# Optimization experiments

Hardware: AMD Instinct MI355X
Metric: run time of the kernel (lower is better)

## Reference

```python
import jax, jax.numpy as jnp
from jax import lax
import numpy as np

N_T = 70            # linspace(0, 60, 70) RK4 grid
STATE_DIM = 12
NOISE_STD = 0.01
T0 = jnp.linspace(0.0, 60.0, N_T)
DEFAULT_TIMES = jnp.array([0, 2, 4, 6, 8, 10, 12, 14, 16, 18, 20, 25, 30, 40, 50, 60], dtype=jnp.float32)
EPORA_DATA = jnp.array([0.01713, 0.145, 0.2442, 0.7659, 1.0, 0.8605, 0.7829, 0.5705,
                        0.6217, 0.331, 0.3388, 0.3116, 0.05062, 0.02504, 0.01163, 0.01163], dtype=jnp.float32)
PARAM_SHIFT = jnp.array([0.5, 0.05, 4.0], dtype=jnp.float32)
PARAM_SCALE = jnp.array([2.5, 0.15, 6.0], dtype=jnp.float32)


def _deriv(x, k1, k2, tau, E):
    # x: [B, 12]; k1,k2,tau: [B]; E: scalar EpoRA(t)
    x1, x2, x3 = x[:, 0], x[:, 1], x[:, 2]
    q1, q2, q3, q4, q5, q6, q7, out = (x[:, 4], x[:, 5], x[:, 6], x[:, 7],
                                       x[:, 8], x[:, 9], x[:, 10], x[:, 11])
    r = 8.0 / tau
    return jnp.stack([
        -k1 * x1 * E + k2 * out,
        -x2 * x2 + k1 * x1 * E,
        -k2 * x3 + x2 * x2,
        -k2 * out + k2 * x3,
        r * (x3 - q1),
        r * (q1 - q2),
        r * (q2 - q3),
        r * (q3 - q4),
        r * (q4 - q5),
        r * (q5 - q6),
        r * (q6 - q7),
        r * (q7 - out),
    ], axis=1)


def _simulate(ps):
    # ps: [B, 3] transformed parameters -> trajectory [N_T, B, 12]
    B = ps.shape[0]
    k1, k2, tau = ps[:, 0], ps[:, 1], ps[:, 2]
    dt = T0[1] - T0[0]
    t_start = T0[:-1]
    # EpoRA is a function of t only: precompute at the 3 RK4 stage times per step
    e_lo = jnp.interp(t_start, DEFAULT_TIMES, EPORA_DATA)
    e_mid = jnp.interp(t_start + 0.5 * dt, DEFAULT_TIMES, EPORA_DATA)
    e_hi = jnp.interp(t_start + dt, DEFAULT_TIMES, EPORA_DATA)
    x0 = jnp.zeros((B, STATE_DIM), dtype=ps.dtype).at[:, 0].set(3.71)

    def step(x, es):
        ea, eb, ec = es
        s1 = _deriv(x, k1, k2, tau, ea)
        s2 = _deriv(x + 0.5 * dt * s1, k1, k2, tau, eb)
        s3 = _deriv(x + 0.5 * dt * s2, k1, k2, tau, eb)
        s4 = _deriv(x + dt * s3, k1, k2, tau, ec)
        xn = x + (dt / 6.0) * (s1 + 2.0 * s2 + 2.0 * s3 + s4)
        return xn, xn

    _, traj = lax.scan(step, x0, (e_lo, e_mid, e_hi))
    return jnp.concatenate([x0[None], traj], axis=0)  # [70, B, 12]


def _forward(parameters, design):
    ps = PARAM_SHIFT + jax.scipy.stats.norm.cdf(parameters) * PARAM_SCALE  # [B,3]
    sol = _simulate(ps)                                   # [70, B, 12]
    y1 = 0.33 * (sol[:, :, 1] + sol[:, :, 2]).T           # [B, 70]
    y2 = 0.26 * (sol[:, :, 0] + sol[:, :, 1] + sol[:, :, 2]).T
    interp = jax.vmap(lambda yb: jnp.interp(design, T0, yb))
    return jnp.concatenate([interp(y1), interp(y2)], axis=1)  # [B, 2*obs_dim]


def setup_inputs() -> dict:
    key = jax.random.key(0)
    k1, k2, k3 = jax.random.split(key, 3)
    B, OBS = 65536, 8
    parameters = jax.random.normal(k1, (B, 3), dtype=jnp.float32)
    design = jnp.sort(60.0 * jax.random.uniform(k2, (OBS,), dtype=jnp.float32))
    noise = jax.random.normal(k3, (B, 2 * OBS), dtype=jnp.float32)
    return {"parameters": parameters, "design": design, "noise": noise}


def reference(parameters, design, noise):
    true_obs = _forward(parameters, design)
    noised_obs = true_obs + NOISE_STD * noise
    return true_obs, noised_obs
```

## Files before the change

kernel.cpp:

```cpp
#include <hip/hip_runtime.h>
#include <math.h>

#define NSTEP 69
#define OBS 8

namespace {

constexpr float kDT = 60.0f / 69.0f;

constexpr float interp_e(float t) {
    constexpr float DTm[16] = {0.f,2.f,4.f,6.f,8.f,10.f,12.f,14.f,16.f,18.f,20.f,25.f,30.f,40.f,50.f,60.f};
    constexpr float EP[16]  = {0.01713f,0.145f,0.2442f,0.7659f,1.0f,0.8605f,0.7829f,0.5705f,
                               0.6217f,0.331f,0.3388f,0.3116f,0.05062f,0.02504f,0.01163f,0.01163f};
    if (t >= 60.0f) return EP[15];
    if (t <= 0.0f)  return EP[0];
    int k = 0;
    for (int m = 0; m < 15; m++) if (t >= DTm[m]) k = m;
    float u = (t - DTm[k]) / (DTm[k + 1] - DTm[k]);
    return EP[k] + u * (EP[k + 1] - EP[k]);
}

struct EQuad { float lo, mid, hi, pad; };
struct ETab4 { EQuad q[NSTEP + 1]; };

constexpr ETab4 make_etab4() {
    ETab4 e{};
    for (int s = 0; s < NSTEP; s++) {
        float t0 = (float)s * kDT;
        e.q[s].lo  = interp_e(t0);
        e.q[s].mid = interp_e(t0 + 0.5f * kDT);
        e.q[s].hi  = interp_e(t0 + kDT);
        e.q[s].pad = 0.0f;
    }
    e.q[NSTEP] = e.q[NSTEP - 1];
    return e;
}

}

__constant__ ETab4 ETAB4 = make_etab4();

template <int CTRL>
__device__ __forceinline__ float qperm(float x) {
    return __int_as_float(
        __builtin_amdgcn_mov_dpp(__float_as_int(x), CTRL, 0xf, 0xf, true));
}
#define QP_SHIFT 0x90
#define QP_BC3   0xFF

__global__ __launch_bounds__(256, 4) void stats5_kernel(
    const float* __restrict__ params,
    const float* __restrict__ design,
    const float* __restrict__ noise,
    float* __restrict__ out,
    int B)
{
    int tid = blockIdx.x * blockDim.x + threadIdx.x;
    int b   = tid >> 2;
    int p   = threadIdx.x & 3;
    if (b >= B) return;
    const bool isL0 = (p == 0);

    int ij[OBS], ij1[OBS]; float wj[OBS], w1j[OBS];
    #pragma unroll
    for (int j = 0; j < OBS; j++) {
        float pos = design[j] * (1.0f / kDT);
        int i = (int)pos;
        i = i < 0 ? 0 : (i > NSTEP - 1 ? NSTEP - 1 : i);
        float w = pos - (float)i;
        ij[j]  = __builtin_amdgcn_readfirstlane(i);
        ij1[j] = ij[j] + 1;
        int wb = __builtin_amdgcn_readfirstlane(__float_as_int(w));
        wj[j]  = __int_as_float(wb);
        w1j[j] = 1.0f - wj[j];
    }

    unsigned long long m_lo = 0ull, m_hi = 0ull;
    #pragma unroll
    for (int j = 0; j < OBS; j++) {
        if (ij[j]  < 64) m_lo |= 1ull << ij[j];  else m_hi |= 1ull << (ij[j]  - 64);
        if (ij1[j] < 64) m_lo |= 1ull << ij1[j]; else m_hi |= 1ull << (ij1[j] - 64);
    }

    float p0 = params[3 * b], p1 = params[3 * b + 1], p2 = params[3 * b + 2];
    const float INV_SQRT2 = 0.7071067811865476f;
    float k1  = fmaf(0.5f * erfcf(-p0 * INV_SQRT2), 2.5f,  0.5f);
    float k2  = fmaf(0.5f * erfcf(-p1 * INV_SQRT2), 0.15f, 0.05f);
    float tau = fmaf(0.5f * erfcf(-p2 * INV_SQRT2), 6.0f,  4.0f);
    float r   = 8.0f / tau;

    const float hdt = 0.5f * kDT;
    const float c6  = kDT * (1.0f / 6.0f);
    const float k2r = 0.125f * k2 * tau;
    const float crh = hdt * r;
    const float crf = kDT * r;
    const float c6r = c6 * r;

    long long base = (long long)b * 16;
    long long nb   = (long long)B * 16;
    float4 nmy = ((const float4*)(noise + base))[p];

    float a12[OBS], a0[OBS], b12[OBS], b0[OBS];
    #pragma unroll
    for (int j = 0; j < OBS; j++) { a12[j] = 0.f; a0[j] = 0.f; b12[j] = 0.f; b0[j] = 0.f; }

    float x0 = 3.71f, x1 = 0.f, x2 = 0.f;
    float WL = 0.f, WH = 0.f;

    if (m_lo & 1ull) {
        #pragma unroll
        for (int j = 0; j < OBS; j++)
            if (ij[j] == 0) { a12[j] = 0.f; a0[j] = 3.71f; }
    }

    auto DERIV = [&](float k1E, float X0, float X1, float X2, float VL, float VH,
                     float& D0, float& D1, float& D2, float& GL, float& GH) {
        float vprev = qperm<QP_SHIFT>(VH);
        float wout  = qperm<QP_BC3>(VH);
        float prev  = isL0 ? (r * X2) : vprev;
        float a  = k1E * X0;
        float sq = X1 * X1;
        D0 = fmaf(k2r, wout, -a);
        D1 = a - sq;
        D2 = fmaf(-k2, X2, sq);
        GL = prev - VL;
        GH = VL - VH;
    };

    const float4* et = reinterpret_cast<const float4*>(&ETAB4.q[0].lo);
    float4 eC = et[0];

    #pragma unroll 1
    for (int s = 0; s < NSTEP; s++) {
        float4 eN = et[s + 1];
        const float ea = eC.x, eb = eC.y, ec = eC.z;
        float k1a = k1 * ea, k1b = k1 * eb, k1c = k1 * ec;

        float d10, d11, d12, G1L, G1H;
        DERIV(k1a, x0, x1, x2, WL, WH, d10, d11, d12, G1L, G1H);
        float t0 = fmaf(hdt, d10, x0);
        float t1 = fmaf(hdt, d11, x1);
        float t2 = fmaf(hdt, d12, x2);
        float UL = fmaf(crh, G1L, WL);
        float UH = fmaf(crh, G1H, WH);

        float d20, d21, d22, G2L, G2H;
        DERIV(k1b, t0, t1, t2, UL, UH, d20, d21, d22, G2L, G2H);
        float ax0 = fmaf(2.0f, d20, d10);
        float ax1 = fmaf(2.0f, d21, d11);
        float ax2 = fmaf(2.0f, d22, d12);
        float AL  = fmaf(2.0f, G2L, G1L);
        float AH  = fmaf(2.0f, G2H, G1H);
        t0 = fmaf(hdt, d20, x0);
        t1 = fmaf(hdt, d21, x1);
        t2 = fmaf(hdt, d22, x2);
        UL = fmaf(crh, G2L, WL);
        UH = fmaf(crh, G2H, WH);

        float d30, d31, d32, G3L, G3H;
        DERIV(k1b, t0, t1, t2, UL, UH, d30, d31, d32, G3L, G3H);
        ax0 = fmaf(2.0f, d30, ax0);
        ax1 = fmaf(2.0f, d31, ax1);
        ax2 = fmaf(2.0f, d32, ax2);
        AL  = fmaf(2.0f, G3L, AL);
        AH  = fmaf(2.0f, G3H, AH);
        t0 = fmaf(kDT, d30, x0);
        t1 = fmaf(kDT, d31, x1);
        t2 = fmaf(kDT, d32, x2);
        UL = fmaf(crf, G3L, WL);
        UH = fmaf(crf, G3H, WH);

        float d40, d41, d42, G4L, G4H;
        DERIV(k1c, t0, t1, t2, UL, UH, d40, d41, d42, G4L, G4H);
        ax0 += d40; ax1 += d41; ax2 += d42;
        x0 = fmaf(c6, ax0, x0);
        x1 = fmaf(c6, ax1, x1);
        x2 = fmaf(c6, ax2, x2);
        AL += G4L; AH += G4H;
        WL = fmaf(c6r, AL, WL);
        WH = fmaf(c6r, AH, WH);

        const int ti = s + 1;
        unsigned long long mm = (ti < 64) ? (m_lo >> ti) : (m_hi >> (ti - 64));
        if (__builtin_expect((int)(mm & 1ull), 0)) {
            float s12 = x1 + x2;
            #pragma unroll
            for (int j = 0; j < OBS; j++) {
                if (ti == ij[j])  { a12[j] = s12; a0[j] = x0; }
                if (ti == ij1[j]) { b12[j] = s12; b0[j] = x0; }
            }
        }
        eC = eN;
    }

    float o1[OBS], o2[OBS];
    #pragma unroll
    for (int j = 0; j < OBS; j++) {
        o1[j] = 0.33f * fmaf(w1j[j], a12[j], wj[j] * b12[j]);
        o2[j] = 0.26f * fmaf(w1j[j], a0[j] + a12[j], wj[j] * (b0[j] + b12[j]));
    }

    float4 v0 = make_float4(o1[0], o1[1], o1[2], o1[3]);
    float4 v1 = make_float4(o1[4], o1[5], o1[6], o1[7]);
    float4 v2 = make_float4(o2[0], o2[1], o2[2], o2[3]);
    float4 v3 = make_float4(o2[4], o2[5], o2[6], o2[7]);

    float4 mine = (p == 0) ? v0 : (p == 1) ? v1 : (p == 2) ? v2 : v3;

    ((float4*)(out + base))[p] = mine;
    ((float4*)(out + nb + base))[p] =
        make_float4(fmaf(0.01f, nmy.x, mine.x), fmaf(0.01f, nmy.y, mine.y),
                    fmaf(0.01f, nmy.z, mine.z), fmaf(0.01f, nmy.w, mine.w));
}

extern "C" void kernel_launch(void* const* d_in, const int* in_sizes, int n_in,
                              void* d_out, int out_size, void* d_ws, size_t ws_size,
                              hipStream_t stream) {
    const float* params = (const float*)d_in[0];
    const float* design = (const float*)d_in[1];
    const float* noise  = (const float*)d_in[2];
    float* out = (float*)d_out;
    int B = in_sizes[0] / 3;
    int block = 256;
    long long threads = (long long)B * 4;
    int grid = (int)((threads + block - 1) / block);
    stats5_kernel<<<grid, block, 0, stream>>>(params, design, noise, out, B);
}
```

Before: 102.1 us.

## Split each sample's delay chain across two lanes instead of four

Each batch element now uses 2 lanes instead of 4. Each lane holds 4 delay-chain states, and the DPP permutations are adjusted to pass the boundary value between lanes and broadcast the output state. This halves the redundant per-lane work on x0..x2, the parameter setup and the interpolation bookkeeping, and halves the thread count. The cost is more registers per thread and fewer waves overall, so there is less latency hiding, and launch bounds drop to 2 blocks.

```diff
diff --git a/kernel.cpp b/kernel.cpp
--- a/kernel.cpp
+++ b/kernel.cpp
@@ -45,10 +45,10 @@
     return __int_as_float(
         __builtin_amdgcn_mov_dpp(__float_as_int(x), CTRL, 0xf, 0xf, true));
 }
-#define QP_SHIFT 0x90
-#define QP_BC3   0xFF
-
-__global__ __launch_bounds__(256, 4) void stats5_kernel(
+#define QP_PREV 0xA0
+#define QP_OUT  0xF5
+
+__global__ __launch_bounds__(256, 2) void stats5_kernel(
     const float* __restrict__ params,
     const float* __restrict__ design,
     const float* __restrict__ noise,
@@ -56,10 +56,10 @@
     int B)
 {
     int tid = blockIdx.x * blockDim.x + threadIdx.x;
-    int b   = tid >> 2;
-    int p   = threadIdx.x & 3;
+    int b   = tid >> 1;
+    int p   = threadIdx.x & 1;
     if (b >= B) return;
-    const bool isL0 = (p == 0);
+    const bool isOdd = (p != 0);
 
     int ij[OBS], ij1[OBS]; float wj[OBS], w1j[OBS];
     #pragma unroll
@@ -98,14 +98,15 @@
 
     long long base = (long long)b * 16;
     long long nb   = (long long)B * 16;
-    float4 nmy = ((const float4*)(noise + base))[p];
+    const float4* nz = (const float4*)(noise + base);
+    float4 nA = nz[2 * p], nB = nz[2 * p + 1];
 
     float a12[OBS], a0[OBS], b12[OBS], b0[OBS];
     #pragma unroll
     for (int j = 0; j < OBS; j++) { a12[j] = 0.f; a0[j] = 0.f; b12[j] = 0.f; b0[j] = 0.f; }
 
     float x0 = 3.71f, x1 = 0.f, x2 = 0.f;
-    float WL = 0.f, WH = 0.f;
+    float W0 = 0.f, W1 = 0.f, W2 = 0.f, W3 = 0.f;
 
     if (m_lo & 1ull) {
         #pragma unroll
@@ -113,18 +114,22 @@
             if (ij[j] == 0) { a12[j] = 0.f; a0[j] = 3.71f; }
     }
 
-    auto DERIV = [&](float k1E, float X0, float X1, float X2, float VL, float VH,
-                     float& D0, float& D1, float& D2, float& GL, float& GH) {
-        float vprev = qperm<QP_SHIFT>(VH);
-        float wout  = qperm<QP_BC3>(VH);
-        float prev  = isL0 ? (r * X2) : vprev;
+    auto DERIV = [&](float k1E, float X0, float X1, float X2,
+                     float V0, float V1, float V2, float V3,
+                     float& D0, float& D1, float& D2,
+                     float& G0, float& G1, float& G2, float& G3) {
+        float vprev = qperm<QP_PREV>(V3);
+        float wout  = qperm<QP_OUT>(V3);
+        float prev  = isOdd ? vprev : (r * X2);
         float a  = k1E * X0;
         float sq = X1 * X1;
         D0 = fmaf(k2r, wout, -a);
         D1 = a - sq;
         D2 = fmaf(-k2, X2, sq);
-        GL = prev - VL;
-        GH = VL - VH;
+        G0 = prev - V0;
+        G1 = V0 - V1;
+        G2 = V1 - V2;
+        G3 = V2 - V3;
     };
 
     const float4* et = reinterpret_cast<const float4*>(&ETAB4.q[0].lo);
@@ -136,49 +141,61 @@
         const float ea = eC.x, eb = eC.y, ec = eC.z;
         float k1a = k1 * ea, k1b = k1 * eb, k1c = k1 * ec;
 
-        float d10, d11, d12, G1L, G1H;
-        DERIV(k1a, x0, x1, x2, WL, WH, d10, d11, d12, G1L, G1H);
+        float d10, d11, d12, G10, G11, G12, G13;
+        DERIV(k1a, x0, x1, x2, W0, W1, W2, W3, d10, d11, d12, G10, G11, G12, G13);
         float t0 = fmaf(hdt, d10, x0);
         float t1 = fmaf(hdt, d11, x1);
         float t2 = fmaf(hdt, d12, x2);
-        float UL = fmaf(crh, G1L, WL);
-        float UH = fmaf(crh, G1H, WH);
-
-        float d20, d21, d22, G2L, G2H;
-        DERIV(k1b, t0, t1, t2, UL, UH, d20, d21, d22, G2L, G2H);
+        float U0 = fmaf(crh, G10, W0);
+        float U1 = fmaf(crh, G11, W1);
+        float U2 = fmaf(crh, G12, W2);
+        float U3 = fmaf(crh, G13, W3);
+
+        float d20, d21, d22, G20, G21, G22, G23;
+        DERIV(k1b, t0, t1, t2, U0, U1, U2, U3, d20, d21, d22, G20, G21, G22, G23);
         float ax0 = fmaf(2.0f, d20, d10);
         float ax1 = fmaf(2.0f, d21, d11);
         float ax2 = fmaf(2.0f, d22, d12);
-        float AL  = fmaf(2.0f, G2L, G1L);
-        float AH  = fmaf(2.0f, G2H, G1H);
+        float A0  = fmaf(2.0f, G20, G10);
+        float A1  = fmaf(2.0f, G21, G11);
+        float A2  = fmaf(2.0f, G22, G12);
+        float A3  = fmaf(2.0f, G23, G13);
         t0 = fmaf(hdt, d20, x0);
         t1 = fmaf(hdt, d21, x1);
         t2 = fmaf(hdt, d22, x2);
-        UL = fmaf(crh, G2L, WL);
-        UH = fmaf(crh, G2H, WH);
-
-        float d30, d31, d32, G3L, G3H;
-        DERIV(k1b, t0, t1, t2, UL, UH, d30, d31, d32, G3L, G3H);
+        U0 = fmaf(crh, G20, W0);
+        U1 = fmaf(crh, G21, W1);
+        U2 = fmaf(crh, G22, W2);
+        U3 = fmaf(crh, G23, W3);
+
+        float d30, d31, d32, G30, G31, G32, G33;
+        DERIV(k1b, t0, t1, t2, U0, U1, U2, U3, d30, d31, d32, G30, G31, G32, G33);
         ax0 = fmaf(2.0f, d30, ax0);
         ax1 = fmaf(2.0f, d31, ax1);
         ax2 = fmaf(2.0f, d32, ax2);
-        AL  = fmaf(2.0f, G3L, AL);
-        AH  = fmaf(2.0f, G3H, AH);
+        A0  = fmaf(2.0f, G30, A0);
+        A1  = fmaf(2.0f, G31, A1);
+        A2  = fmaf(2.0f, G32, A2);
+        A3  = fmaf(2.0f, G33, A3);
         t0 = fmaf(kDT, d30, x0);
         t1 = fmaf(kDT, d31, x1);
         t2 = fmaf(kDT, d32, x2);
-        UL = fmaf(crf, G3L, WL);
-        UH = fmaf(crf, G3H, WH);
-
-        float d40, d41, d42, G4L, G4H;
-        DERIV(k1c, t0, t1, t2, UL, UH, d40, d41, d42, G4L, G4H);
+        U0 = fmaf(crf, G30, W0);
+        U1 = fmaf(crf, G31, W1);
+        U2 = fmaf(crf, G32, W2);
+        U3 = fmaf(crf, G33, W3);
+
+        float d40, d41, d42, G40, G41, G42, G43;
+        DERIV(k1c, t0, t1, t2, U0, U1, U2, U3, d40, d41, d42, G40, G41, G42, G43);
         ax0 += d40; ax1 += d41; ax2 += d42;
         x0 = fmaf(c6, ax0, x0);
         x1 = fmaf(c6, ax1, x1);
         x2 = fmaf(c6, ax2, x2);
-        AL += G4L; AH += G4H;
-        WL = fmaf(c6r, AL, WL);
-        WH = fmaf(c6r, AH, WH);
+        A0 += G40; A1 += G41; A2 += G42; A3 += G43;
+        W0 = fmaf(c6r, A0, W0);
+        W1 = fmaf(c6r, A1, W1);
+        W2 = fmaf(c6r, A2, W2);
+        W3 = fmaf(c6r, A3, W3);
 
         const int ti = s + 1;
         unsigned long long mm = (ti < 64) ? (m_lo >> ti) : (m_hi >> (ti - 64));
@@ -205,12 +222,17 @@
     float4 v2 = make_float4(o2[0], o2[1], o2[2], o2[3]);
     float4 v3 = make_float4(o2[4], o2[5], o2[6], o2[7]);
 
-    float4 mine = (p == 0) ? v0 : (p == 1) ? v1 : (p == 2) ? v2 : v3;
-
-    ((float4*)(out + base))[p] = mine;
-    ((float4*)(out + nb + base))[p] =
-        make_float4(fmaf(0.01f, nmy.x, mine.x), fmaf(0.01f, nmy.y, mine.y),
-                    fmaf(0.01f, nmy.z, mine.z), fmaf(0.01f, nmy.w, mine.w));
+    float4 mA = p ? v2 : v0;
+    float4 mB = p ? v3 : v1;
+
+    float4* outv = (float4*)(out + base);
+    float4* outn = (float4*)(out + nb + base);
+    outv[2 * p]     = mA;
+    outv[2 * p + 1] = mB;
+    outn[2 * p]     = make_float4(fmaf(0.01f, nA.x, mA.x), fmaf(0.01f, nA.y, mA.y),
+                                  fmaf(0.01f, nA.z, mA.z), fmaf(0.01f, nA.w, mA.w));
+    outn[2 * p + 1] = make_float4(fmaf(0.01f, nB.x, mB.x), fmaf(0.01f, nB.y, mB.y),
+                                  fmaf(0.01f, nB.z, mB.z), fmaf(0.01f, nB.w, mB.w));
 }
 
 extern "C" void kernel_launch(void* const* d_in, const int* in_sizes, int n_in,
@@ -222,7 +244,7 @@
     float* out = (float*)d_out;
     int B = in_sizes[0] / 3;
     int block = 256;
-    long long threads = (long long)B * 4;
+    long long threads = (long long)B * 2;
     int grid = (int)((threads + block - 1) / block);
     stats5_kernel<<<grid, block, 0, stream>>>(params, design, noise, out, B);
 }
```

New measurement: 88.08 us. -13.7%, faster.
